# Performance work log

Measured on AMD Instinct MI355X. Metric: run time of the kernel, lower is better.

Reference implementation:

```python
import jax, jax.numpy as jnp
import numpy as np

B, S, D = 2, 2048, 2048
E, TOP_K, H = 8, 2, 1024
HS = 2048  # shared expert ffn dim


def setup_inputs() -> dict:
    key = jax.random.key(0)
    ks = jax.random.split(key, 8)
    sc_d = 1.0 / np.sqrt(D)
    sc_h = 1.0 / np.sqrt(H)
    sc_hs = 1.0 / np.sqrt(HS)
    return {
        "hidden_states": jax.random.normal(ks[0], (B, S, D), jnp.float32),
        "router_w": jax.random.normal(ks[1], (D, E), jnp.float32) * sc_d,
        "w_gate": jax.random.normal(ks[2], (E, D, H), jnp.float32) * sc_d,
        "w_up": jax.random.normal(ks[3], (E, D, H), jnp.float32) * sc_d,
        "w_down": jax.random.normal(ks[4], (E, H, D), jnp.float32) * sc_h,
        "sw_gate": jax.random.normal(ks[5], (D, HS), jnp.float32) * sc_d,
        "sw_up": jax.random.normal(ks[6], (D, HS), jnp.float32) * sc_d,
        "sw_down": jax.random.normal(ks[7], (HS, D), jnp.float32) * sc_hs,
    }


def reference(hidden_states, router_w, w_gate, w_up, w_down, sw_gate, sw_up, sw_down):
    b, s, d = hidden_states.shape
    x = hidden_states.reshape(-1, d)  # [T, D]
    T = x.shape[0]

    # --- gate: softmax router + top-k, renormalized weights ---
    logits = x @ router_w                         # [T, E]
    probs = jax.nn.softmax(logits, axis=-1)
    topk_w, topk_idx = jax.lax.top_k(probs, TOP_K)  # [T, K]
    topk_w = topk_w / jnp.sum(topk_w, axis=-1, keepdims=True)

    # --- routed experts (SwiGLU), dense all-expert compute + sparse combine ---
    g = jnp.einsum('td,edh->teh', x, w_gate)
    u = jnp.einsum('td,edh->teh', x, w_up)
    h = jax.nn.silu(g) * u                        # [T, E, H]
    y = jnp.einsum('teh,ehd->ted', h, w_down)     # [T, E, D]

    # combine weights: scatter top-k weights into [T, E]
    combine = jnp.zeros((T, E), dtype=x.dtype)
    combine = combine.at[jnp.arange(T)[:, None], topk_idx].add(topk_w)
    routed = jnp.einsum('te,ted->td', combine, y)  # [T, D]

    # --- shared expert (SwiGLU) on residual stream ---
    sh = jax.nn.silu(hidden_states @ sw_gate) * (hidden_states @ sw_up)
    shared = sh @ sw_down                          # [B, S, D]

    return routed.reshape(b, s, d) + shared
```

## Files before the change

### kernel.cpp

```cpp
#include <hip/hip_runtime.h>

#define T_TOK 4096
#define DDIM  2048
#define NEXP  8
#define HDIM  1024
#define HSDIM 2048
#define NASSIGN 8192
#define MAXTILES 72

typedef __attribute__((ext_vector_type(8))) short bf16x8;
typedef __attribute__((ext_vector_type(4))) float f32x4;

__device__ __forceinline__ ushort f2bf(float f) {
  union { float f; unsigned u; } v; v.f = f;
  unsigned r = v.u + 0x7FFFu + ((v.u >> 16) & 1u);
  return (ushort)(r >> 16);
}

__device__ __forceinline__ void gload16(const void* g, void* s) {
  __builtin_amdgcn_global_load_lds((const __attribute__((address_space(1))) void*)g,
                                   (__attribute__((address_space(3))) void*)s, 16, 0, 0);
}


__global__ void zero_k(int* ctl) {
  int i = threadIdx.x;
#pragma unroll
  for (int j = 0; j < 4; ++j) ctl[i + j * 256] = 0;
}

__global__ void router_k(const float* __restrict__ x, const float* __restrict__ rw,
                         int* __restrict__ ctl, int* __restrict__ tidx,
                         float* __restrict__ twt) {
  int t = blockIdx.x;
  int lane = threadIdx.x;
  const float* xr = x + (size_t)t * DDIM;
  float acc[NEXP];
#pragma unroll
  for (int e = 0; e < NEXP; ++e) acc[e] = 0.f;
  for (int d0 = lane * 4; d0 < DDIM; d0 += 256) {
    float4 xv = *(const float4*)(xr + d0);
    const float* rwp = rw + (size_t)d0 * NEXP;
#pragma unroll
    for (int e = 0; e < NEXP; ++e)
      acc[e] += xv.x * rwp[e] + xv.y * rwp[NEXP + e] +
                xv.z * rwp[2 * NEXP + e] + xv.w * rwp[3 * NEXP + e];
  }
#pragma unroll
  for (int e = 0; e < NEXP; ++e) {
#pragma unroll
    for (int off = 32; off >= 1; off >>= 1) acc[e] += __shfl_xor(acc[e], off, 64);
  }
  if (lane == 0) {
    int i0 = 0; float m0 = acc[0];
#pragma unroll
    for (int e = 1; e < NEXP; ++e) if (acc[e] > m0) { m0 = acc[e]; i0 = e; }
    int i1 = -1; float m1 = -3.4e38f;
#pragma unroll
    for (int e = 0; e < NEXP; ++e) if (e != i0 && acc[e] > m1) { m1 = acc[e]; i1 = e; }
    float w0 = 1.f / (1.f + __expf(m1 - m0));
    float w1 = 1.f - w0;
    tidx[2 * t] = i0;     twt[2 * t] = w0;
    tidx[2 * t + 1] = i1; twt[2 * t + 1] = w1;
    atomicAdd(&ctl[8 + i0], 1);
    atomicAdd(&ctl[8 + i1], 1);
  }
}

__global__ void plan_k(int* ctl) {
  if (threadIdx.x != 0 || blockIdx.x != 0) return;
  int off = 0, nt = 0;
  for (int e = 0; e < NEXP; ++e) {
    int c = ctl[8 + e];
    ctl[24 + e] = off;
    ctl[16 + e] = off;
    int ntile = (c + 127) >> 7;
    for (int j = 0; j < ntile; ++j) {
      ctl[64 + nt] = e;
      ctl[160 + nt] = off + j * 128;
      ctl[256 + nt] = off + c;
      ++nt;
    }
    off += c;
  }
  ctl[24 + NEXP] = off;
  ctl[0] = nt;
}

__global__ void scatter_k(const int* __restrict__ tidx, const float* __restrict__ twt,
                          int* __restrict__ ctl, int* __restrict__ stok,
                          float* __restrict__ swt) {
  int t = blockIdx.x * blockDim.x + threadIdx.x;
  if (t >= T_TOK) return;
#pragma unroll
  for (int k = 0; k < 2; ++k) {
    int e = tidx[2 * t + k];
    int p = atomicAdd(&ctl[16 + e], 1);
    stok[p] = t;
    swt[p] = twt[2 * t + k];
  }
}

__global__ void cvt_k(const float* __restrict__ in, ushort* __restrict__ out) {
  long long i = ((long long)blockIdx.x * blockDim.x + threadIdx.x) * 8;
  float4 a = *(const float4*)(in + i);
  float4 b = *(const float4*)(in + i + 4);
  ushort4 o0 = { f2bf(a.x), f2bf(a.y), f2bf(a.z), f2bf(a.w) };
  ushort4 o1 = { f2bf(b.x), f2bf(b.y), f2bf(b.z), f2bf(b.w) };
  *(ushort4*)(out + i) = o0;
  *(ushort4*)(out + i + 4) = o1;
}

__global__ void tcvt_k(const float* __restrict__ in, ushort* __restrict__ out,
                       int R, int C) {
  __shared__ float tile[64][65];
  in  += (size_t)blockIdx.z * R * C;
  out += (size_t)blockIdx.z * R * C;
  int c0 = blockIdx.x * 64, r0 = blockIdx.y * 64;
  int tx = threadIdx.x & 15, ty = threadIdx.x >> 4;
#pragma unroll
  for (int i = 0; i < 4; ++i) {
    float4 v = *(const float4*)(in + (size_t)(r0 + ty + 16 * i) * C + c0 + tx * 4);
    tile[ty + 16 * i][tx * 4 + 0] = v.x;
    tile[ty + 16 * i][tx * 4 + 1] = v.y;
    tile[ty + 16 * i][tx * 4 + 2] = v.z;
    tile[ty + 16 * i][tx * 4 + 3] = v.w;
  }
  __syncthreads();
#pragma unroll
  for (int i = 0; i < 4; ++i) {
    ushort4 o = { f2bf(tile[tx * 4 + 0][ty + 16 * i]),
                  f2bf(tile[tx * 4 + 1][ty + 16 * i]),
                  f2bf(tile[tx * 4 + 2][ty + 16 * i]),
                  f2bf(tile[tx * 4 + 3][ty + 16 * i]) };
    *(ushort4*)(out + (size_t)(c0 + ty + 16 * i) * R + r0 + tx * 4) = o;
  }
}

template <bool ROUTED>
__global__ __launch_bounds__(256, 2) void gateup_k(
    const ushort* __restrict__ Ax, const ushort* __restrict__ BgT,
    const ushort* __restrict__ BuT, ushort* __restrict__ Hout,
    const int* __restrict__ ctl, const int* __restrict__ stok, int N) {
  __shared__ ushort As[128 * 32];
  __shared__ ushort Bgs[128 * 32];
  __shared__ ushort Bus[128 * 32];
  __shared__ int toks[128];

  int tid = threadIdx.x;
  int row0, nrows;
  const ushort *Bg, *Bu;
  if (ROUTED) {
    if (blockIdx.x >= ctl[0]) return;
    row0 = ctl[160 + blockIdx.x];
    int end = ctl[256 + blockIdx.x];
    nrows = end - row0; if (nrows > 128) nrows = 128;
    size_t es = (size_t)ctl[64 + blockIdx.x] * HDIM * DDIM;
    Bg = BgT + es; Bu = BuT + es;
    if (tid < 128) toks[tid] = (tid < nrows) ? stok[row0 + tid] : 0;
  } else {
    row0 = blockIdx.x * 128; nrows = 128;
    Bg = BgT; Bu = BuT;
    if (tid < 128) toks[tid] = row0 + tid;
  }
  int col0 = blockIdx.y * 128;
  __syncthreads();

  int srow = tid >> 2, skc = tid & 3;
  const ushort* aS0 = Ax + (size_t)toks[srow] * DDIM + skc * 8;
  const ushort* aS1 = Ax + (size_t)toks[64 + srow] * DDIM + skc * 8;
  const ushort* bgS0 = Bg + (size_t)(col0 + srow) * DDIM + skc * 8;
  const ushort* bgS1 = Bg + (size_t)(col0 + 64 + srow) * DDIM + skc * 8;
  const ushort* buS0 = Bu + (size_t)(col0 + srow) * DDIM + skc * 8;
  const ushort* buS1 = Bu + (size_t)(col0 + 64 + srow) * DDIM + skc * 8;
  ushort* aD0 = As + tid * 8;   ushort* aD1 = As + (256 + tid) * 8;
  ushort* bgD0 = Bgs + tid * 8; ushort* bgD1 = Bgs + (256 + tid) * 8;
  ushort* buD0 = Bus + tid * 8; ushort* buD1 = Bus + (256 + tid) * 8;

  int lane = tid & 63, w = tid >> 6;
  int g = lane >> 4, r16 = lane & 15;
  int wr = (w >> 1) * 64, wc = (w & 1) * 64;

  f32x4 accg[4][4], accu[4][4];
  f32x4 z = {0.f, 0.f, 0.f, 0.f};
#pragma unroll
  for (int i = 0; i < 4; ++i)
#pragma unroll
    for (int j = 0; j < 4; ++j) { accg[i][j] = z; accu[i][j] = z; }

  for (int k0 = 0; k0 < DDIM; k0 += 32) {
    gload16(aS0 + k0, aD0);   gload16(aS1 + k0, aD1);
    gload16(bgS0 + k0, bgD0); gload16(bgS1 + k0, bgD1);
    gload16(buS0 + k0, buD0); gload16(buS1 + k0, buD1);
    __syncthreads();
    bf16x8 af[4], bgf[4], buf_[4];
#pragma unroll
    for (int mf = 0; mf < 4; ++mf)
      af[mf] = *(const bf16x8*)(As + (wr + mf * 16 + r16) * 32 + g * 8);
#pragma unroll
    for (int nf = 0; nf < 4; ++nf) {
      bgf[nf] = *(const bf16x8*)(Bgs + (wc + nf * 16 + r16) * 32 + g * 8);
      buf_[nf] = *(const bf16x8*)(Bus + (wc + nf * 16 + r16) * 32 + g * 8);
    }
#pragma unroll
    for (int mf = 0; mf < 4; ++mf)
#pragma unroll
      for (int nf = 0; nf < 4; ++nf) {
        accg[mf][nf] = __builtin_amdgcn_mfma_f32_16x16x32_bf16(af[mf], bgf[nf], accg[mf][nf], 0, 0, 0);
        accu[mf][nf] = __builtin_amdgcn_mfma_f32_16x16x32_bf16(af[mf], buf_[nf], accu[mf][nf], 0, 0, 0);
      }
    __syncthreads();
  }

#pragma unroll
  for (int mf = 0; mf < 4; ++mf) {
#pragma unroll
    for (int j = 0; j < 4; ++j) {
      int rloc = wr + mf * 16 + g * 4 + j;
      if (rloc < nrows) {
        size_t obase = (size_t)(row0 + rloc) * N + col0 + wc;
#pragma unroll
        for (int nf = 0; nf < 4; ++nf) {
          float gv = accg[mf][nf][j];
          float uv = accu[mf][nf][j];
          float hv = gv / (1.f + __expf(-gv)) * uv;
          Hout[obase + nf * 16 + r16] = f2bf(hv);
        }
      }
    }
  }
}

template <bool ROUTED>
__global__ __launch_bounds__(256, 2) void down_k(
    const ushort* __restrict__ Ah, const ushort* __restrict__ BdT,
    float* __restrict__ Out, const int* __restrict__ ctl,
    const int* __restrict__ stok, const float* __restrict__ swt, int Ktot) {
  __shared__ ushort As[128 * 32];
  __shared__ ushort Bs[128 * 32];
  __shared__ int tokl[128];
  __shared__ float wtl[128];

  int tid = threadIdx.x;
  int row0, nrows;
  const ushort* Bd;
  if (ROUTED) {
    if (blockIdx.x >= ctl[0]) return;
    row0 = ctl[160 + blockIdx.x];
    int end = ctl[256 + blockIdx.x];
    nrows = end - row0; if (nrows > 128) nrows = 128;
    Bd = BdT + (size_t)ctl[64 + blockIdx.x] * DDIM * HDIM;
    if (tid < 128) {
      bool v = tid < nrows;
      tokl[tid] = v ? stok[row0 + tid] : 0;
      wtl[tid] = v ? swt[row0 + tid] : 0.f;
    }
  } else {
    row0 = blockIdx.x * 128; nrows = 128;
    Bd = BdT;
  }
  int col0 = blockIdx.y * 128;
  __syncthreads();

  int srow = tid >> 2, skc = tid & 3;
  const ushort* aS0 = Ah + (size_t)(row0 + srow) * Ktot + skc * 8;
  const ushort* aS1 = Ah + (size_t)(row0 + 64 + srow) * Ktot + skc * 8;
  const ushort* bS0 = Bd + (size_t)(col0 + srow) * Ktot + skc * 8;
  const ushort* bS1 = Bd + (size_t)(col0 + 64 + srow) * Ktot + skc * 8;
  ushort* aD0 = As + tid * 8; ushort* aD1 = As + (256 + tid) * 8;
  ushort* bD0 = Bs + tid * 8; ushort* bD1 = Bs + (256 + tid) * 8;

  int lane = tid & 63, w = tid >> 6;
  int g = lane >> 4, r16 = lane & 15;
  int wr = (w >> 1) * 64, wc = (w & 1) * 64;

  f32x4 acc[4][4];
  f32x4 z = {0.f, 0.f, 0.f, 0.f};
#pragma unroll
  for (int i = 0; i < 4; ++i)
#pragma unroll
    for (int j = 0; j < 4; ++j) acc[i][j] = z;

  for (int k0 = 0; k0 < Ktot; k0 += 32) {
    gload16(aS0 + k0, aD0); gload16(aS1 + k0, aD1);
    gload16(bS0 + k0, bD0); gload16(bS1 + k0, bD1);
    __syncthreads();
    bf16x8 af[4], bf[4];
#pragma unroll
    for (int mf = 0; mf < 4; ++mf)
      af[mf] = *(const bf16x8*)(As + (wr + mf * 16 + r16) * 32 + g * 8);
#pragma unroll
    for (int nf = 0; nf < 4; ++nf)
      bf[nf] = *(const bf16x8*)(Bs + (wc + nf * 16 + r16) * 32 + g * 8);
#pragma unroll
    for (int mf = 0; mf < 4; ++mf)
#pragma unroll
      for (int nf = 0; nf < 4; ++nf)
        acc[mf][nf] = __builtin_amdgcn_mfma_f32_16x16x32_bf16(af[mf], bf[nf], acc[mf][nf], 0, 0, 0);
    __syncthreads();
  }

#pragma unroll
  for (int mf = 0; mf < 4; ++mf) {
#pragma unroll
    for (int j = 0; j < 4; ++j) {
      int rloc = wr + mf * 16 + g * 4 + j;
      if (rloc < nrows) {
        if (ROUTED) {
          int t = tokl[rloc];
          float wt = wtl[rloc];
          size_t obase = (size_t)t * DDIM + col0 + wc;
#pragma unroll
          for (int nf = 0; nf < 4; ++nf)
            atomicAdd(&Out[obase + nf * 16 + r16], wt * acc[mf][nf][j]);
        } else {
          size_t obase = (size_t)(row0 + rloc) * DDIM + col0 + wc;
#pragma unroll
          for (int nf = 0; nf < 4; ++nf)
            Out[obase + nf * 16 + r16] = acc[mf][nf][j];
        }
      }
    }
  }
}

extern "C" void kernel_launch(void* const* d_in, const int* in_sizes, int n_in,
                              void* d_out, int out_size, void* d_ws, size_t ws_size,
                              hipStream_t stream) {
  const float* x   = (const float*)d_in[0];
  const float* rw  = (const float*)d_in[1];
  const float* wg  = (const float*)d_in[2];
  const float* wu  = (const float*)d_in[3];
  const float* wd  = (const float*)d_in[4];
  const float* swg = (const float*)d_in[5];
  const float* swu = (const float*)d_in[6];
  const float* swd = (const float*)d_in[7];
  float* out = (float*)d_out;

  char* ws = (char*)d_ws;
  size_t off = 0;
  auto alloc = [&](size_t bytes) {
    char* p = ws + off;
    off += (bytes + 4095) & ~(size_t)4095;
    return p;
  };
  int*    ctl   = (int*)alloc(4096);
  int*    tidx  = (int*)alloc(NASSIGN * 4);
  float*  twt   = (float*)alloc(NASSIGN * 4);
  int*    stok  = (int*)alloc(NASSIGN * 4);
  float*  swt_  = (float*)alloc(NASSIGN * 4);
  ushort* xbf   = (ushort*)alloc((size_t)T_TOK * DDIM * 2);
  ushort* wgT   = (ushort*)alloc((size_t)NEXP * HDIM * DDIM * 2);
  ushort* wuT   = (ushort*)alloc((size_t)NEXP * HDIM * DDIM * 2);
  ushort* wdT   = (ushort*)alloc((size_t)NEXP * DDIM * HDIM * 2);
  ushort* swgT  = (ushort*)alloc((size_t)HSDIM * DDIM * 2);
  ushort* swuT  = (ushort*)alloc((size_t)HSDIM * DDIM * 2);
  ushort* swdT  = (ushort*)alloc((size_t)DDIM * HSDIM * 2);
  ushort* hbuf  = (ushort*)alloc((size_t)NASSIGN * HDIM * 2);
  ushort* shbuf = (ushort*)alloc((size_t)T_TOK * HSDIM * 2);
  if (off > ws_size) return;

  zero_k<<<1, 256, 0, stream>>>(ctl);
  router_k<<<T_TOK, 64, 0, stream>>>(x, rw, ctl, tidx, twt);
  plan_k<<<1, 64, 0, stream>>>(ctl);
  scatter_k<<<16, 256, 0, stream>>>(tidx, twt, ctl, stok, swt_);

  cvt_k<<<(T_TOK * DDIM / 8) / 256, 256, 0, stream>>>(x, xbf);
  tcvt_k<<<dim3(HDIM / 64, DDIM / 64, NEXP), 256, 0, stream>>>(wg, wgT, DDIM, HDIM);
  tcvt_k<<<dim3(HDIM / 64, DDIM / 64, NEXP), 256, 0, stream>>>(wu, wuT, DDIM, HDIM);
  tcvt_k<<<dim3(DDIM / 64, HDIM / 64, NEXP), 256, 0, stream>>>(wd, wdT, HDIM, DDIM);
  tcvt_k<<<dim3(HSDIM / 64, DDIM / 64, 1), 256, 0, stream>>>(swg, swgT, DDIM, HSDIM);
  tcvt_k<<<dim3(HSDIM / 64, DDIM / 64, 1), 256, 0, stream>>>(swu, swuT, DDIM, HSDIM);
  tcvt_k<<<dim3(DDIM / 64, HSDIM / 64, 1), 256, 0, stream>>>(swd, swdT, HSDIM, DDIM);

  gateup_k<true><<<dim3(MAXTILES, HDIM / 128), 256, 0, stream>>>(xbf, wgT, wuT, hbuf, ctl, stok, HDIM);
  gateup_k<false><<<dim3(T_TOK / 128, HSDIM / 128), 256, 0, stream>>>(xbf, swgT, swuT, shbuf, ctl, stok, HSDIM);
  down_k<false><<<dim3(T_TOK / 128, DDIM / 128), 256, 0, stream>>>(shbuf, swdT, out, ctl, stok, swt_, HSDIM);
  down_k<true><<<dim3(MAXTILES, DDIM / 128), 256, 0, stream>>>(hbuf, wdT, out, ctl, stok, swt_, HDIM);
}
```

Baseline: 802.8 us.

## Use 256x256 double-buffered GEMM tiles with concatenated gate/up weights and XCD swizzle

Gate and up weights are transposed into one concatenated matrix per expert and for the shared expert. A single wider GEMM then writes raw gate/up outputs, and a separate SiLU kernel combines them. GEMM tiles grow to 256x256 with 512 threads, K=64 steps and double-buffered LDS. An XCD-aware workgroup swizzle is added, and routed tiles are planned in 256-row chunks. This aims to raise data reuse and overlap loads with MFMA work. In exchange it adds an extra HBM round trip through the bf16 GU buffer, uses much more LDS per block, and pads more rows in the routed tiles.

```diff
diff --git a/kernel.cpp b/kernel.cpp
--- a/kernel.cpp
+++ b/kernel.cpp
@@ -6,7 +6,7 @@
 #define HDIM  1024
 #define HSDIM 2048
 #define NASSIGN 8192
-#define MAXTILES 72
+#define MAXTILES 40
 
 typedef __attribute__((ext_vector_type(8))) short bf16x8;
 typedef __attribute__((ext_vector_type(4))) float f32x4;
@@ -16,10 +16,18 @@
   unsigned r = v.u + 0x7FFFu + ((v.u >> 16) & 1u);
   return (ushort)(r >> 16);
 }
-
+__device__ __forceinline__ float bf2f(ushort s) {
+  union { float f; unsigned u; } v; v.u = ((unsigned)s) << 16;
+  return v.f;
+}
 __device__ __forceinline__ void gload16(const void* g, void* s) {
   __builtin_amdgcn_global_load_lds((const __attribute__((address_space(1))) void*)g,
                                    (__attribute__((address_space(3))) void*)s, 16, 0, 0);
+}
+__device__ __forceinline__ int xcd_swz(int orig, int nwg) {
+  int q = nwg >> 3, r = nwg & 7;
+  int xcd = orig & 7, pos = orig >> 3;
+  return (xcd < r ? xcd * (q + 1) : r * (q + 1) + (xcd - r) * q) + pos;
 }
 
 
@@ -74,10 +82,10 @@
     int c = ctl[8 + e];
     ctl[24 + e] = off;
     ctl[16 + e] = off;
-    int ntile = (c + 127) >> 7;
+    int ntile = (c + 255) >> 8;
     for (int j = 0; j < ntile; ++j) {
       ctl[64 + nt] = e;
-      ctl[160 + nt] = off + j * 128;
+      ctl[160 + nt] = off + j * 256;
       ctl[256 + nt] = off + c;
       ++nt;
     }
@@ -112,10 +120,10 @@
 }
 
 __global__ void tcvt_k(const float* __restrict__ in, ushort* __restrict__ out,
-                       int R, int C) {
+                       int R, int C, long long inZ, long long outZ) {
   __shared__ float tile[64][65];
-  in  += (size_t)blockIdx.z * R * C;
-  out += (size_t)blockIdx.z * R * C;
+  in  += (size_t)blockIdx.z * inZ;
+  out += (size_t)blockIdx.z * outZ;
   int c0 = blockIdx.x * 64, r0 = blockIdx.y * 64;
   int tx = threadIdx.x & 15, ty = threadIdx.x >> 4;
 #pragma unroll
@@ -137,142 +145,260 @@
   }
 }
 
+__global__ void silu_k(const ushort* __restrict__ gu, ushort* __restrict__ h, int N) {
+  int row = blockIdx.x, c = threadIdx.x * 8;
+  const ushort* gp = gu + (size_t)row * 2 * N;
+  bf16x8 gv = *(const bf16x8*)(gp + c);
+  bf16x8 uv = *(const bf16x8*)(gp + N + c);
+  ushort o[8];
+#pragma unroll
+  for (int k = 0; k < 8; ++k) {
+    float gf = bf2f((ushort)gv[k]);
+    float uf = bf2f((ushort)uv[k]);
+    float hv = gf / (1.f + __expf(-gf)) * uf;
+    o[k] = f2bf(hv);
+  }
+  ushort4 o0 = { o[0], o[1], o[2], o[3] };
+  ushort4 o1 = { o[4], o[5], o[6], o[7] };
+  *(ushort4*)(h + (size_t)row * N + c) = o0;
+  *(ushort4*)(h + (size_t)row * N + c + 4) = o1;
+}
+
 template <bool ROUTED>
-__global__ __launch_bounds__(256, 2) void gateup_k(
-    const ushort* __restrict__ Ax, const ushort* __restrict__ BgT,
-    const ushort* __restrict__ BuT, ushort* __restrict__ Hout,
-    const int* __restrict__ ctl, const int* __restrict__ stok, int N) {
-  __shared__ ushort As[128 * 32];
-  __shared__ ushort Bgs[128 * 32];
-  __shared__ ushort Bus[128 * 32];
-  __shared__ int toks[128];
+__global__ __launch_bounds__(512, 2) void gucat_k(
+    const ushort* __restrict__ Ax, const ushort* __restrict__ Bcat,
+    ushort* __restrict__ GU, const int* __restrict__ ctl,
+    const int* __restrict__ stok, int Ncat) {
+  __shared__ ushort As[2][256 * 64];
+  __shared__ ushort Bs[2][256 * 64];
+  __shared__ int toks[256];
+
+  int nwg = gridDim.x * gridDim.y;
+  int wg = xcd_swz(blockIdx.y * gridDim.x + blockIdx.x, nwg);
+  int mt = wg % gridDim.x, ntt = wg / gridDim.x;
 
   int tid = threadIdx.x;
   int row0, nrows;
-  const ushort *Bg, *Bu;
+  const ushort* Bp;
   if (ROUTED) {
-    if (blockIdx.x >= ctl[0]) return;
-    row0 = ctl[160 + blockIdx.x];
-    int end = ctl[256 + blockIdx.x];
-    nrows = end - row0; if (nrows > 128) nrows = 128;
-    size_t es = (size_t)ctl[64 + blockIdx.x] * HDIM * DDIM;
-    Bg = BgT + es; Bu = BuT + es;
-    if (tid < 128) toks[tid] = (tid < nrows) ? stok[row0 + tid] : 0;
+    if (mt >= ctl[0]) return;
+    row0 = ctl[160 + mt];
+    int end = ctl[256 + mt];
+    nrows = end - row0; if (nrows > 256) nrows = 256;
+    Bp = Bcat + (size_t)ctl[64 + mt] * (2048 * 2048);
+    if (tid < 256) toks[tid] = (tid < nrows) ? stok[row0 + tid] : 0;
   } else {
-    row0 = blockIdx.x * 128; nrows = 128;
-    Bg = BgT; Bu = BuT;
-    if (tid < 128) toks[tid] = row0 + tid;
-  }
-  int col0 = blockIdx.y * 128;
+    row0 = mt * 256; nrows = 256;
+    Bp = Bcat;
+    if (tid < 256) toks[tid] = row0 + tid;
+  }
+  int col0 = ntt * 256;
   __syncthreads();
 
-  int srow = tid >> 2, skc = tid & 3;
-  const ushort* aS0 = Ax + (size_t)toks[srow] * DDIM + skc * 8;
-  const ushort* aS1 = Ax + (size_t)toks[64 + srow] * DDIM + skc * 8;
-  const ushort* bgS0 = Bg + (size_t)(col0 + srow) * DDIM + skc * 8;
-  const ushort* bgS1 = Bg + (size_t)(col0 + 64 + srow) * DDIM + skc * 8;
-  const ushort* buS0 = Bu + (size_t)(col0 + srow) * DDIM + skc * 8;
-  const ushort* buS1 = Bu + (size_t)(col0 + 64 + srow) * DDIM + skc * 8;
-  ushort* aD0 = As + tid * 8;   ushort* aD1 = As + (256 + tid) * 8;
-  ushort* bgD0 = Bgs + tid * 8; ushort* bgD1 = Bgs + (256 + tid) * 8;
-  ushort* buD0 = Bus + tid * 8; ushort* buD1 = Bus + (256 + tid) * 8;
+  int srow = tid >> 3, skc = (tid & 7) * 8;
+  const ushort* aSrc[4];
+  const ushort* bSrc[4];
+#pragma unroll
+  for (int rr = 0; rr < 4; ++rr) {
+    aSrc[rr] = Ax + (size_t)toks[rr * 64 + srow] * DDIM + skc;
+    bSrc[rr] = Bp + (size_t)(col0 + rr * 64 + srow) * DDIM + skc;
+  }
 
   int lane = tid & 63, w = tid >> 6;
   int g = lane >> 4, r16 = lane & 15;
-  int wr = (w >> 1) * 64, wc = (w & 1) * 64;
-
-  f32x4 accg[4][4], accu[4][4];
+  int wrow = (w >> 2) * 128, wcol = (w & 3) * 64;
+
+  f32x4 acc[8][4];
   f32x4 z = {0.f, 0.f, 0.f, 0.f};
 #pragma unroll
-  for (int i = 0; i < 4; ++i)
-#pragma unroll
-    for (int j = 0; j < 4; ++j) { accg[i][j] = z; accu[i][j] = z; }
-
-  for (int k0 = 0; k0 < DDIM; k0 += 32) {
-    gload16(aS0 + k0, aD0);   gload16(aS1 + k0, aD1);
-    gload16(bgS0 + k0, bgD0); gload16(bgS1 + k0, bgD1);
-    gload16(buS0 + k0, buD0); gload16(buS1 + k0, buD1);
+  for (int i = 0; i < 8; ++i)
+#pragma unroll
+    for (int j = 0; j < 4; ++j) acc[i][j] = z;
+
+#define STAGE_GU(buf, k0)                                          \
+  {                                                                 \
+    _Pragma("unroll")                                               \
+    for (int rr = 0; rr < 4; ++rr) {                                \
+      gload16(aSrc[rr] + (k0), &As[buf][(rr * 512 + tid) * 8]);     \
+      gload16(bSrc[rr] + (k0), &Bs[buf][(rr * 512 + tid) * 8]);     \
+    }                                                               \
+  }
+#define COMPUTE_GU(buf)                                                              \
+  {                                                                                   \
+    _Pragma("unroll")                                                                 \
+    for (int kk = 0; kk < 2; ++kk) {                                                  \
+      bf16x8 af[8], bf_[4];                                                           \
+      _Pragma("unroll")                                                               \
+      for (int mf = 0; mf < 8; ++mf)                                                  \
+        af[mf] = *(const bf16x8*)(&As[buf][(wrow + mf * 16 + r16) * 64 + kk * 32 + g * 8]); \
+      _Pragma("unroll")                                                               \
+      for (int nf = 0; nf < 4; ++nf)                                                  \
+        bf_[nf] = *(const bf16x8*)(&Bs[buf][(wcol + nf * 16 + r16) * 64 + kk * 32 + g * 8]); \
+      _Pragma("unroll")                                                               \
+      for (int mf = 0; mf < 8; ++mf)                                                  \
+        _Pragma("unroll")                                                             \
+        for (int nf = 0; nf < 4; ++nf)                                                \
+          acc[mf][nf] = __builtin_amdgcn_mfma_f32_16x16x32_bf16(af[mf], bf_[nf], acc[mf][nf], 0, 0, 0); \
+    }                                                                                 \
+  }
+
+  STAGE_GU(0, 0);
+  __syncthreads();
+  int cur = 0;
+  for (int k0 = 64; k0 < DDIM; k0 += 64) {
+    STAGE_GU(cur ^ 1, k0);
+    COMPUTE_GU(cur);
     __syncthreads();
-    bf16x8 af[4], bgf[4], buf_[4];
-#pragma unroll
-    for (int mf = 0; mf < 4; ++mf)
-      af[mf] = *(const bf16x8*)(As + (wr + mf * 16 + r16) * 32 + g * 8);
-#pragma unroll
-    for (int nf = 0; nf < 4; ++nf) {
-      bgf[nf] = *(const bf16x8*)(Bgs + (wc + nf * 16 + r16) * 32 + g * 8);
-      buf_[nf] = *(const bf16x8*)(Bus + (wc + nf * 16 + r16) * 32 + g * 8);
-    }
-#pragma unroll
-    for (int mf = 0; mf < 4; ++mf)
-#pragma unroll
-      for (int nf = 0; nf < 4; ++nf) {
-        accg[mf][nf] = __builtin_amdgcn_mfma_f32_16x16x32_bf16(af[mf], bgf[nf], accg[mf][nf], 0, 0, 0);
-        accu[mf][nf] = __builtin_amdgcn_mfma_f32_16x16x32_bf16(af[mf], buf_[nf], accu[mf][nf], 0, 0, 0);
-      }
-    __syncthreads();
-  }
-
-#pragma unroll
-  for (int mf = 0; mf < 4; ++mf) {
+    cur ^= 1;
+  }
+  COMPUTE_GU(cur);
+
+#pragma unroll
+  for (int mf = 0; mf < 8; ++mf) {
 #pragma unroll
     for (int j = 0; j < 4; ++j) {
-      int rloc = wr + mf * 16 + g * 4 + j;
+      int rloc = wrow + mf * 16 + g * 4 + j;
       if (rloc < nrows) {
-        size_t obase = (size_t)(row0 + rloc) * N + col0 + wc;
-#pragma unroll
-        for (int nf = 0; nf < 4; ++nf) {
-          float gv = accg[mf][nf][j];
-          float uv = accu[mf][nf][j];
-          float hv = gv / (1.f + __expf(-gv)) * uv;
-          Hout[obase + nf * 16 + r16] = f2bf(hv);
-        }
+        size_t ob = (size_t)(row0 + rloc) * Ncat + col0 + wcol;
+#pragma unroll
+        for (int nf = 0; nf < 4; ++nf)
+          GU[ob + nf * 16 + r16] = f2bf(acc[mf][nf][j]);
       }
     }
   }
-}
-
-template <bool ROUTED>
-__global__ __launch_bounds__(256, 2) void down_k(
+#undef STAGE_GU
+#undef COMPUTE_GU
+}
+
+__global__ __launch_bounds__(512, 2) void downR_k(
     const ushort* __restrict__ Ah, const ushort* __restrict__ BdT,
     float* __restrict__ Out, const int* __restrict__ ctl,
-    const int* __restrict__ stok, const float* __restrict__ swt, int Ktot) {
-  __shared__ ushort As[128 * 32];
-  __shared__ ushort Bs[128 * 32];
-  __shared__ int tokl[128];
-  __shared__ float wtl[128];
+    const int* __restrict__ stok, const float* __restrict__ swt) {
+  __shared__ ushort As[2][256 * 64];
+  __shared__ ushort Bs[2][256 * 64];
+  __shared__ int tokl[256];
+  __shared__ float wtl[256];
+
+  int nwg = gridDim.x * gridDim.y;
+  int wg = xcd_swz(blockIdx.y * gridDim.x + blockIdx.x, nwg);
+  int mt = wg % gridDim.x, ntt = wg / gridDim.x;
 
   int tid = threadIdx.x;
-  int row0, nrows;
-  const ushort* Bd;
-  if (ROUTED) {
-    if (blockIdx.x >= ctl[0]) return;
-    row0 = ctl[160 + blockIdx.x];
-    int end = ctl[256 + blockIdx.x];
-    nrows = end - row0; if (nrows > 128) nrows = 128;
-    Bd = BdT + (size_t)ctl[64 + blockIdx.x] * DDIM * HDIM;
-    if (tid < 128) {
-      bool v = tid < nrows;
-      tokl[tid] = v ? stok[row0 + tid] : 0;
-      wtl[tid] = v ? swt[row0 + tid] : 0.f;
-    }
-  } else {
-    row0 = blockIdx.x * 128; nrows = 128;
-    Bd = BdT;
-  }
-  int col0 = blockIdx.y * 128;
+  if (mt >= ctl[0]) return;
+  int row0 = ctl[160 + mt];
+  int end = ctl[256 + mt];
+  int nrows = end - row0; if (nrows > 256) nrows = 256;
+  const ushort* Bp = BdT + (size_t)ctl[64 + mt] * (2048 * 1024);
+  if (tid < 256) {
+    bool v = tid < nrows;
+    tokl[tid] = v ? stok[row0 + tid] : 0;
+    wtl[tid] = v ? swt[row0 + tid] : 0.f;
+  }
+  int col0 = ntt * 256;
   __syncthreads();
 
-  int srow = tid >> 2, skc = tid & 3;
-  const ushort* aS0 = Ah + (size_t)(row0 + srow) * Ktot + skc * 8;
-  const ushort* aS1 = Ah + (size_t)(row0 + 64 + srow) * Ktot + skc * 8;
-  const ushort* bS0 = Bd + (size_t)(col0 + srow) * Ktot + skc * 8;
-  const ushort* bS1 = Bd + (size_t)(col0 + 64 + srow) * Ktot + skc * 8;
-  ushort* aD0 = As + tid * 8; ushort* aD1 = As + (256 + tid) * 8;
-  ushort* bD0 = Bs + tid * 8; ushort* bD1 = Bs + (256 + tid) * 8;
+  int srow = tid >> 3, skc = (tid & 7) * 8;
+  const ushort* aSrc[4];
+  const ushort* bSrc[4];
+#pragma unroll
+  for (int rr = 0; rr < 4; ++rr) {
+    aSrc[rr] = Ah + (size_t)(row0 + rr * 64 + srow) * HDIM + skc;
+    bSrc[rr] = Bp + (size_t)(col0 + rr * 64 + srow) * HDIM + skc;
+  }
 
   int lane = tid & 63, w = tid >> 6;
   int g = lane >> 4, r16 = lane & 15;
-  int wr = (w >> 1) * 64, wc = (w & 1) * 64;
+  int wrow = (w >> 2) * 128, wcol = (w & 3) * 64;
+
+  f32x4 acc[8][4];
+  f32x4 z = {0.f, 0.f, 0.f, 0.f};
+#pragma unroll
+  for (int i = 0; i < 8; ++i)
+#pragma unroll
+    for (int j = 0; j < 4; ++j) acc[i][j] = z;
+
+#define STAGE_DR(buf, k0)                                          \
+  {                                                                 \
+    _Pragma("unroll")                                               \
+    for (int rr = 0; rr < 4; ++rr) {                                \
+      gload16(aSrc[rr] + (k0), &As[buf][(rr * 512 + tid) * 8]);     \
+      gload16(bSrc[rr] + (k0), &Bs[buf][(rr * 512 + tid) * 8]);     \
+    }                                                               \
+  }
+#define COMPUTE_DR(buf)                                                              \
+  {                                                                                   \
+    _Pragma("unroll")                                                                 \
+    for (int kk = 0; kk < 2; ++kk) {                                                  \
+      bf16x8 af[8], bf_[4];                                                           \
+      _Pragma("unroll")                                                               \
+      for (int mf = 0; mf < 8; ++mf)                                                  \
+        af[mf] = *(const bf16x8*)(&As[buf][(wrow + mf * 16 + r16) * 64 + kk * 32 + g * 8]); \
+      _Pragma("unroll")                                                               \
+      for (int nf = 0; nf < 4; ++nf)                                                  \
+        bf_[nf] = *(const bf16x8*)(&Bs[buf][(wcol + nf * 16 + r16) * 64 + kk * 32 + g * 8]); \
+      _Pragma("unroll")                                                               \
+      for (int mf = 0; mf < 8; ++mf)                                                  \
+        _Pragma("unroll")                                                             \
+        for (int nf = 0; nf < 4; ++nf)                                                \
+          acc[mf][nf] = __builtin_amdgcn_mfma_f32_16x16x32_bf16(af[mf], bf_[nf], acc[mf][nf], 0, 0, 0); \
+    }                                                                                 \
+  }
+
+  STAGE_DR(0, 0);
+  __syncthreads();
+  int cur = 0;
+  for (int k0 = 64; k0 < HDIM; k0 += 64) {
+    STAGE_DR(cur ^ 1, k0);
+    COMPUTE_DR(cur);
+    __syncthreads();
+    cur ^= 1;
+  }
+  COMPUTE_DR(cur);
+
+#pragma unroll
+  for (int mf = 0; mf < 8; ++mf) {
+#pragma unroll
+    for (int j = 0; j < 4; ++j) {
+      int rloc = wrow + mf * 16 + g * 4 + j;
+      if (rloc < nrows) {
+        int t = tokl[rloc];
+        float wt = wtl[rloc];
+        size_t ob = (size_t)t * DDIM + col0 + wcol;
+#pragma unroll
+        for (int nf = 0; nf < 4; ++nf)
+          atomicAdd(&Out[ob + nf * 16 + r16], wt * acc[mf][nf][j]);
+      }
+    }
+  }
+#undef STAGE_DR
+#undef COMPUTE_DR
+}
+
+__global__ __launch_bounds__(512, 2) void downS_k(
+    const ushort* __restrict__ Ah, const ushort* __restrict__ BdT,
+    float* __restrict__ Out) {
+  __shared__ ushort As[2][128 * 64];
+  __shared__ ushort Bs[2][256 * 64];
+
+  int nwg = gridDim.x * gridDim.y;
+  int wg = xcd_swz(blockIdx.y * gridDim.x + blockIdx.x, nwg);
+  int mt = wg % gridDim.x, ntt = wg / gridDim.x;
+  int row0 = mt * 128, col0 = ntt * 256;
+
+  int tid = threadIdx.x;
+  int srow = tid >> 3, skc = (tid & 7) * 8;
+  const ushort* aSrc[2];
+  const ushort* bSrc[4];
+#pragma unroll
+  for (int rr = 0; rr < 2; ++rr)
+    aSrc[rr] = Ah + (size_t)(row0 + rr * 64 + srow) * HSDIM + skc;
+#pragma unroll
+  for (int rr = 0; rr < 4; ++rr)
+    bSrc[rr] = BdT + (size_t)(col0 + rr * 64 + srow) * HSDIM + skc;
+
+  int lane = tid & 63, w = tid >> 6;
+  int g = lane >> 4, r16 = lane & 15;
+  int wrow = (w >> 2) * 64, wcol = (w & 3) * 64;
 
   f32x4 acc[4][4];
   f32x4 z = {0.f, 0.f, 0.f, 0.f};
@@ -281,47 +407,58 @@
 #pragma unroll
     for (int j = 0; j < 4; ++j) acc[i][j] = z;
 
-  for (int k0 = 0; k0 < Ktot; k0 += 32) {
-    gload16(aS0 + k0, aD0); gload16(aS1 + k0, aD1);
-    gload16(bS0 + k0, bD0); gload16(bS1 + k0, bD1);
+#define STAGE_DS(buf, k0)                                          \
+  {                                                                 \
+    _Pragma("unroll")                                               \
+    for (int rr = 0; rr < 2; ++rr)                                  \
+      gload16(aSrc[rr] + (k0), &As[buf][(rr * 512 + tid) * 8]);     \
+    _Pragma("unroll")                                               \
+    for (int rr = 0; rr < 4; ++rr)                                  \
+      gload16(bSrc[rr] + (k0), &Bs[buf][(rr * 512 + tid) * 8]);     \
+  }
+#define COMPUTE_DS(buf)                                                              \
+  {                                                                                   \
+    _Pragma("unroll")                                                                 \
+    for (int kk = 0; kk < 2; ++kk) {                                                  \
+      bf16x8 af[4], bf_[4];                                                           \
+      _Pragma("unroll")                                                               \
+      for (int mf = 0; mf < 4; ++mf)                                                  \
+        af[mf] = *(const bf16x8*)(&As[buf][(wrow + mf * 16 + r16) * 64 + kk * 32 + g * 8]); \
+      _Pragma("unroll")                                                               \
+      for (int nf = 0; nf < 4; ++nf)                                                  \
+        bf_[nf] = *(const bf16x8*)(&Bs[buf][(wcol + nf * 16 + r16) * 64 + kk * 32 + g * 8]); \
+      _Pragma("unroll")                                                               \
+      for (int mf = 0; mf < 4; ++mf)                                                  \
+        _Pragma("unroll")                                                             \
+        for (int nf = 0; nf < 4; ++nf)                                                \
+          acc[mf][nf] = __builtin_amdgcn_mfma_f32_16x16x32_bf16(af[mf], bf_[nf], acc[mf][nf], 0, 0, 0); \
+    }                                                                                 \
+  }
+
+  STAGE_DS(0, 0);
+  __syncthreads();
+  int cur = 0;
+  for (int k0 = 64; k0 < HSDIM; k0 += 64) {
+    STAGE_DS(cur ^ 1, k0);
+    COMPUTE_DS(cur);
     __syncthreads();
-    bf16x8 af[4], bf[4];
-#pragma unroll
-    for (int mf = 0; mf < 4; ++mf)
-      af[mf] = *(const bf16x8*)(As + (wr + mf * 16 + r16) * 32 + g * 8);
-#pragma unroll
-    for (int nf = 0; nf < 4; ++nf)
-      bf[nf] = *(const bf16x8*)(Bs + (wc + nf * 16 + r16) * 32 + g * 8);
-#pragma unroll
-    for (int mf = 0; mf < 4; ++mf)
+    cur ^= 1;
+  }
+  COMPUTE_DS(cur);
+
+#pragma unroll
+  for (int mf = 0; mf < 4; ++mf) {
+#pragma unroll
+    for (int j = 0; j < 4; ++j) {
+      int rloc = wrow + mf * 16 + g * 4 + j;
+      size_t ob = (size_t)(row0 + rloc) * DDIM + col0 + wcol;
 #pragma unroll
       for (int nf = 0; nf < 4; ++nf)
-        acc[mf][nf] = __builtin_amdgcn_mfma_f32_16x16x32_bf16(af[mf], bf[nf], acc[mf][nf], 0, 0, 0);
-    __syncthreads();
-  }
-
-#pragma unroll
-  for (int mf = 0; mf < 4; ++mf) {
-#pragma unroll
-    for (int j = 0; j < 4; ++j) {
-      int rloc = wr + mf * 16 + g * 4 + j;
-      if (rloc < nrows) {
-        if (ROUTED) {
-          int t = tokl[rloc];
-          float wt = wtl[rloc];
-          size_t obase = (size_t)t * DDIM + col0 + wc;
-#pragma unroll
-          for (int nf = 0; nf < 4; ++nf)
-            atomicAdd(&Out[obase + nf * 16 + r16], wt * acc[mf][nf][j]);
-        } else {
-          size_t obase = (size_t)(row0 + rloc) * DDIM + col0 + wc;
-#pragma unroll
-          for (int nf = 0; nf < 4; ++nf)
-            Out[obase + nf * 16 + r16] = acc[mf][nf][j];
-        }
-      }
+        Out[ob + nf * 16 + r16] = acc[mf][nf][j];
     }
   }
+#undef STAGE_DS
+#undef COMPUTE_DS
 }
 
 extern "C" void kernel_launch(void* const* d_in, const int* in_sizes, int n_in,
@@ -350,14 +487,14 @@
   int*    stok  = (int*)alloc(NASSIGN * 4);
   float*  swt_  = (float*)alloc(NASSIGN * 4);
   ushort* xbf   = (ushort*)alloc((size_t)T_TOK * DDIM * 2);
-  ushort* wgT   = (ushort*)alloc((size_t)NEXP * HDIM * DDIM * 2);
-  ushort* wuT   = (ushort*)alloc((size_t)NEXP * HDIM * DDIM * 2);
+  ushort* catR  = (ushort*)alloc((size_t)NEXP * 2048 * 2048 * 2);
   ushort* wdT   = (ushort*)alloc((size_t)NEXP * DDIM * HDIM * 2);
-  ushort* swgT  = (ushort*)alloc((size_t)HSDIM * DDIM * 2);
-  ushort* swuT  = (ushort*)alloc((size_t)HSDIM * DDIM * 2);
+  ushort* catS  = (ushort*)alloc((size_t)2 * HSDIM * DDIM * 2);
   ushort* swdT  = (ushort*)alloc((size_t)DDIM * HSDIM * 2);
-  ushort* hbuf  = (ushort*)alloc((size_t)NASSIGN * HDIM * 2);
-  ushort* shbuf = (ushort*)alloc((size_t)T_TOK * HSDIM * 2);
+  ushort* GU    = (ushort*)alloc((size_t)NASSIGN * 2048 * 2);
+  ushort* hr    = (ushort*)alloc((size_t)(NASSIGN + 256) * HDIM * 2);
+  ushort* hs    = (ushort*)alloc((size_t)T_TOK * HSDIM * 2);
+  (void)alloc(1 << 20);
   if (off > ws_size) return;
 
   zero_k<<<1, 256, 0, stream>>>(ctl);
@@ -366,15 +503,24 @@
   scatter_k<<<16, 256, 0, stream>>>(tidx, twt, ctl, stok, swt_);
 
   cvt_k<<<(T_TOK * DDIM / 8) / 256, 256, 0, stream>>>(x, xbf);
-  tcvt_k<<<dim3(HDIM / 64, DDIM / 64, NEXP), 256, 0, stream>>>(wg, wgT, DDIM, HDIM);
-  tcvt_k<<<dim3(HDIM / 64, DDIM / 64, NEXP), 256, 0, stream>>>(wu, wuT, DDIM, HDIM);
-  tcvt_k<<<dim3(DDIM / 64, HDIM / 64, NEXP), 256, 0, stream>>>(wd, wdT, HDIM, DDIM);
-  tcvt_k<<<dim3(HSDIM / 64, DDIM / 64, 1), 256, 0, stream>>>(swg, swgT, DDIM, HSDIM);
-  tcvt_k<<<dim3(HSDIM / 64, DDIM / 64, 1), 256, 0, stream>>>(swu, swuT, DDIM, HSDIM);
-  tcvt_k<<<dim3(DDIM / 64, HSDIM / 64, 1), 256, 0, stream>>>(swd, swdT, HSDIM, DDIM);
-
-  gateup_k<true><<<dim3(MAXTILES, HDIM / 128), 256, 0, stream>>>(xbf, wgT, wuT, hbuf, ctl, stok, HDIM);
-  gateup_k<false><<<dim3(T_TOK / 128, HSDIM / 128), 256, 0, stream>>>(xbf, swgT, swuT, shbuf, ctl, stok, HSDIM);
-  down_k<false><<<dim3(T_TOK / 128, DDIM / 128), 256, 0, stream>>>(shbuf, swdT, out, ctl, stok, swt_, HSDIM);
-  down_k<true><<<dim3(MAXTILES, DDIM / 128), 256, 0, stream>>>(hbuf, wdT, out, ctl, stok, swt_, HDIM);
-}
+  tcvt_k<<<dim3(HDIM / 64, DDIM / 64, NEXP), 256, 0, stream>>>(
+      wg, catR, DDIM, HDIM, (long long)DDIM * HDIM, 2048LL * 2048);
+  tcvt_k<<<dim3(HDIM / 64, DDIM / 64, NEXP), 256, 0, stream>>>(
+      wu, catR + 1024 * 2048, DDIM, HDIM, (long long)DDIM * HDIM, 2048LL * 2048);
+  tcvt_k<<<dim3(DDIM / 64, HDIM / 64, NEXP), 256, 0, stream>>>(
+      wd, wdT, HDIM, DDIM, (long long)HDIM * DDIM, 2048LL * 1024);
+  tcvt_k<<<dim3(HSDIM / 64, DDIM / 64, 1), 256, 0, stream>>>(
+      swg, catS, DDIM, HSDIM, 0, 0);
+  tcvt_k<<<dim3(HSDIM / 64, DDIM / 64, 1), 256, 0, stream>>>(
+      swu, catS + 2048 * 2048, DDIM, HSDIM, 0, 0);
+  tcvt_k<<<dim3(DDIM / 64, HSDIM / 64, 1), 256, 0, stream>>>(
+      swd, swdT, HSDIM, DDIM, 0, 0);
+
+  gucat_k<true><<<dim3(MAXTILES, 2048 / 256), 512, 0, stream>>>(xbf, catR, GU, ctl, stok, 2048);
+  silu_k<<<NASSIGN, HDIM / 8, 0, stream>>>(GU, hr, HDIM);
+  gucat_k<false><<<dim3(T_TOK / 256, 4096 / 256), 512, 0, stream>>>(xbf, catS, GU, ctl, stok, 4096);
+  silu_k<<<T_TOK, HSDIM / 8, 0, stream>>>(GU, hs, HSDIM);
+
+  downS_k<<<dim3(T_TOK / 128, DDIM / 256), 512, 0, stream>>>(hs, swdT, out);
+  downR_k<<<dim3(MAXTILES, DDIM / 256), 512, 0, stream>>>(hr, wdT, out, ctl, stok, swt_);
+}
```

Result: slower. 923.5 us (+15.0%).

## Double-buffer LDS in GEMMs, swizzle LDS slots, and remap workgroups per XCD

Applied to the files above, without the earlier changes.

The gate/up and down GEMM kernels now use two LDS buffers, so the next K-slice is loaded while the current one is computed, and each iteration needs one barrier instead of two. LDS columns are XOR-swizzled on both the store and the fragment read to cut bank conflicts. Workgroup IDs are remapped so that tiles placed on the same XCD share operands in its L2. down_k's launch bound is raised to 3 waves per SIMD, which puts more pressure on registers, and the double buffers double LDS use.

```diff
diff --git a/kernel.cpp b/kernel.cpp
--- a/kernel.cpp
+++ b/kernel.cpp
@@ -16,10 +16,14 @@
   unsigned r = v.u + 0x7FFFu + ((v.u >> 16) & 1u);
   return (ushort)(r >> 16);
 }
-
 __device__ __forceinline__ void gload16(const void* g, void* s) {
   __builtin_amdgcn_global_load_lds((const __attribute__((address_space(1))) void*)g,
                                    (__attribute__((address_space(3))) void*)s, 16, 0, 0);
+}
+__device__ __forceinline__ int xcd_swz(int orig, int nwg) {
+  int q = nwg >> 3, r = nwg & 7;
+  int xcd = orig & 7, pos = orig >> 3;
+  return (xcd < r ? xcd * (q + 1) : r * (q + 1) + (xcd - r) * q) + pos;
 }
 
 
@@ -112,10 +116,10 @@
 }
 
 __global__ void tcvt_k(const float* __restrict__ in, ushort* __restrict__ out,
-                       int R, int C) {
+                       int R, int C, long long inZ, long long outZ) {
   __shared__ float tile[64][65];
-  in  += (size_t)blockIdx.z * R * C;
-  out += (size_t)blockIdx.z * R * C;
+  in  += (size_t)blockIdx.z * inZ;
+  out += (size_t)blockIdx.z * outZ;
   int c0 = blockIdx.x * 64, r0 = blockIdx.y * 64;
   int tx = threadIdx.x & 15, ty = threadIdx.x >> 4;
 #pragma unroll
@@ -142,43 +146,46 @@
     const ushort* __restrict__ Ax, const ushort* __restrict__ BgT,
     const ushort* __restrict__ BuT, ushort* __restrict__ Hout,
     const int* __restrict__ ctl, const int* __restrict__ stok, int N) {
-  __shared__ ushort As[128 * 32];
-  __shared__ ushort Bgs[128 * 32];
-  __shared__ ushort Bus[128 * 32];
+  __shared__ ushort As[2][128 * 32];
+  __shared__ ushort Bgs[2][128 * 32];
+  __shared__ ushort Bus[2][128 * 32];
   __shared__ int toks[128];
+
+  int nwg = gridDim.x * gridDim.y;
+  int wg = xcd_swz(blockIdx.y * gridDim.x + blockIdx.x, nwg);
+  int mt = wg % gridDim.x, ntt = wg / gridDim.x;
 
   int tid = threadIdx.x;
   int row0, nrows;
   const ushort *Bg, *Bu;
   if (ROUTED) {
-    if (blockIdx.x >= ctl[0]) return;
-    row0 = ctl[160 + blockIdx.x];
-    int end = ctl[256 + blockIdx.x];
+    if (mt >= ctl[0]) return;
+    row0 = ctl[160 + mt];
+    int end = ctl[256 + mt];
     nrows = end - row0; if (nrows > 128) nrows = 128;
-    size_t es = (size_t)ctl[64 + blockIdx.x] * HDIM * DDIM;
+    size_t es = (size_t)ctl[64 + mt] * HDIM * DDIM;
     Bg = BgT + es; Bu = BuT + es;
     if (tid < 128) toks[tid] = (tid < nrows) ? stok[row0 + tid] : 0;
   } else {
-    row0 = blockIdx.x * 128; nrows = 128;
+    row0 = mt * 128; nrows = 128;
     Bg = BgT; Bu = BuT;
     if (tid < 128) toks[tid] = row0 + tid;
   }
-  int col0 = blockIdx.y * 128;
+  int col0 = ntt * 128;
   __syncthreads();
 
-  int srow = tid >> 2, skc = tid & 3;
-  const ushort* aS0 = Ax + (size_t)toks[srow] * DDIM + skc * 8;
-  const ushort* aS1 = Ax + (size_t)toks[64 + srow] * DDIM + skc * 8;
-  const ushort* bgS0 = Bg + (size_t)(col0 + srow) * DDIM + skc * 8;
-  const ushort* bgS1 = Bg + (size_t)(col0 + 64 + srow) * DDIM + skc * 8;
-  const ushort* buS0 = Bu + (size_t)(col0 + srow) * DDIM + skc * 8;
-  const ushort* buS1 = Bu + (size_t)(col0 + 64 + srow) * DDIM + skc * 8;
-  ushort* aD0 = As + tid * 8;   ushort* aD1 = As + (256 + tid) * 8;
-  ushort* bgD0 = Bgs + tid * 8; ushort* bgD1 = Bgs + (256 + tid) * 8;
-  ushort* buD0 = Bus + tid * 8; ushort* buD1 = Bus + (256 + tid) * 8;
+  int srow = tid >> 2;
+  int sslot = (tid & 3) ^ ((tid >> 3) & 3);
+  const ushort* aS0 = Ax + (size_t)toks[srow] * DDIM + sslot * 8;
+  const ushort* aS1 = Ax + (size_t)toks[64 + srow] * DDIM + sslot * 8;
+  const ushort* bgS0 = Bg + (size_t)(col0 + srow) * DDIM + sslot * 8;
+  const ushort* bgS1 = Bg + (size_t)(col0 + 64 + srow) * DDIM + sslot * 8;
+  const ushort* buS0 = Bu + (size_t)(col0 + srow) * DDIM + sslot * 8;
+  const ushort* buS1 = Bu + (size_t)(col0 + 64 + srow) * DDIM + sslot * 8;
 
   int lane = tid & 63, w = tid >> 6;
   int g = lane >> 4, r16 = lane & 15;
+  int xg = (g ^ ((r16 >> 1) & 3)) * 8;
   int wr = (w >> 1) * 64, wc = (w & 1) * 64;
 
   f32x4 accg[4][4], accu[4][4];
@@ -188,29 +195,45 @@
 #pragma unroll
     for (int j = 0; j < 4; ++j) { accg[i][j] = z; accu[i][j] = z; }
 
-  for (int k0 = 0; k0 < DDIM; k0 += 32) {
-    gload16(aS0 + k0, aD0);   gload16(aS1 + k0, aD1);
-    gload16(bgS0 + k0, bgD0); gload16(bgS1 + k0, bgD1);
-    gload16(buS0 + k0, buD0); gload16(buS1 + k0, buD1);
+#define STAGE_GU(buf, k0)                                  \
+  {                                                         \
+    gload16(aS0 + (k0), &As[buf][tid * 8]);                 \
+    gload16(aS1 + (k0), &As[buf][(256 + tid) * 8]);         \
+    gload16(bgS0 + (k0), &Bgs[buf][tid * 8]);               \
+    gload16(bgS1 + (k0), &Bgs[buf][(256 + tid) * 8]);       \
+    gload16(buS0 + (k0), &Bus[buf][tid * 8]);               \
+    gload16(buS1 + (k0), &Bus[buf][(256 + tid) * 8]);       \
+  }
+#define COMPUTE_GU(buf)                                                            \
+  {                                                                                 \
+    bf16x8 af[4], bgf[4], buf_[4];                                                  \
+    _Pragma("unroll")                                                               \
+    for (int mf = 0; mf < 4; ++mf)                                                  \
+      af[mf] = *(const bf16x8*)(&As[buf][(wr + mf * 16 + r16) * 32 + xg]);          \
+    _Pragma("unroll")                                                               \
+    for (int nf = 0; nf < 4; ++nf) {                                                \
+      bgf[nf] = *(const bf16x8*)(&Bgs[buf][(wc + nf * 16 + r16) * 32 + xg]);        \
+      buf_[nf] = *(const bf16x8*)(&Bus[buf][(wc + nf * 16 + r16) * 32 + xg]);       \
+    }                                                                               \
+    _Pragma("unroll")                                                               \
+    for (int mf = 0; mf < 4; ++mf)                                                  \
+      _Pragma("unroll")                                                             \
+      for (int nf = 0; nf < 4; ++nf) {                                              \
+        accg[mf][nf] = __builtin_amdgcn_mfma_f32_16x16x32_bf16(af[mf], bgf[nf], accg[mf][nf], 0, 0, 0); \
+        accu[mf][nf] = __builtin_amdgcn_mfma_f32_16x16x32_bf16(af[mf], buf_[nf], accu[mf][nf], 0, 0, 0); \
+      }                                                                             \
+  }
+
+  STAGE_GU(0, 0);
+  __syncthreads();
+  int cur = 0;
+  for (int k0 = 32; k0 < DDIM; k0 += 32) {
+    STAGE_GU(cur ^ 1, k0);
+    COMPUTE_GU(cur);
     __syncthreads();
-    bf16x8 af[4], bgf[4], buf_[4];
-#pragma unroll
-    for (int mf = 0; mf < 4; ++mf)
-      af[mf] = *(const bf16x8*)(As + (wr + mf * 16 + r16) * 32 + g * 8);
-#pragma unroll
-    for (int nf = 0; nf < 4; ++nf) {
-      bgf[nf] = *(const bf16x8*)(Bgs + (wc + nf * 16 + r16) * 32 + g * 8);
-      buf_[nf] = *(const bf16x8*)(Bus + (wc + nf * 16 + r16) * 32 + g * 8);
-    }
-#pragma unroll
-    for (int mf = 0; mf < 4; ++mf)
-#pragma unroll
-      for (int nf = 0; nf < 4; ++nf) {
-        accg[mf][nf] = __builtin_amdgcn_mfma_f32_16x16x32_bf16(af[mf], bgf[nf], accg[mf][nf], 0, 0, 0);
-        accu[mf][nf] = __builtin_amdgcn_mfma_f32_16x16x32_bf16(af[mf], buf_[nf], accu[mf][nf], 0, 0, 0);
-      }
-    __syncthreads();
-  }
+    cur ^= 1;
+  }
+  COMPUTE_GU(cur);
 
 #pragma unroll
   for (int mf = 0; mf < 4; ++mf) {
@@ -229,49 +252,55 @@
       }
     }
   }
+#undef STAGE_GU
+#undef COMPUTE_GU
 }
 
 template <bool ROUTED>
-__global__ __launch_bounds__(256, 2) void down_k(
+__global__ __launch_bounds__(256, 3) void down_k(
     const ushort* __restrict__ Ah, const ushort* __restrict__ BdT,
     float* __restrict__ Out, const int* __restrict__ ctl,
     const int* __restrict__ stok, const float* __restrict__ swt, int Ktot) {
-  __shared__ ushort As[128 * 32];
-  __shared__ ushort Bs[128 * 32];
+  __shared__ ushort As[2][128 * 32];
+  __shared__ ushort Bs[2][128 * 32];
   __shared__ int tokl[128];
   __shared__ float wtl[128];
+
+  int nwg = gridDim.x * gridDim.y;
+  int wg = xcd_swz(blockIdx.y * gridDim.x + blockIdx.x, nwg);
+  int mt = wg % gridDim.x, ntt = wg / gridDim.x;
 
   int tid = threadIdx.x;
   int row0, nrows;
   const ushort* Bd;
   if (ROUTED) {
-    if (blockIdx.x >= ctl[0]) return;
-    row0 = ctl[160 + blockIdx.x];
-    int end = ctl[256 + blockIdx.x];
+    if (mt >= ctl[0]) return;
+    row0 = ctl[160 + mt];
+    int end = ctl[256 + mt];
     nrows = end - row0; if (nrows > 128) nrows = 128;
-    Bd = BdT + (size_t)ctl[64 + blockIdx.x] * DDIM * HDIM;
+    Bd = BdT + (size_t)ctl[64 + mt] * DDIM * HDIM;
     if (tid < 128) {
       bool v = tid < nrows;
       tokl[tid] = v ? stok[row0 + tid] : 0;
       wtl[tid] = v ? swt[row0 + tid] : 0.f;
     }
   } else {
-    row0 = blockIdx.x * 128; nrows = 128;
+    row0 = mt * 128; nrows = 128;
     Bd = BdT;
   }
-  int col0 = blockIdx.y * 128;
+  int col0 = ntt * 128;
   __syncthreads();
 
-  int srow = tid >> 2, skc = tid & 3;
-  const ushort* aS0 = Ah + (size_t)(row0 + srow) * Ktot + skc * 8;
-  const ushort* aS1 = Ah + (size_t)(row0 + 64 + srow) * Ktot + skc * 8;
-  const ushort* bS0 = Bd + (size_t)(col0 + srow) * Ktot + skc * 8;
-  const ushort* bS1 = Bd + (size_t)(col0 + 64 + srow) * Ktot + skc * 8;
-  ushort* aD0 = As + tid * 8; ushort* aD1 = As + (256 + tid) * 8;
-  ushort* bD0 = Bs + tid * 8; ushort* bD1 = Bs + (256 + tid) * 8;
+  int srow = tid >> 2;
+  int sslot = (tid & 3) ^ ((tid >> 3) & 3);
+  const ushort* aS0 = Ah + (size_t)(row0 + srow) * Ktot + sslot * 8;
+  const ushort* aS1 = Ah + (size_t)(row0 + 64 + srow) * Ktot + sslot * 8;
+  const ushort* bS0 = Bd + (size_t)(col0 + srow) * Ktot + sslot * 8;
+  const ushort* bS1 = Bd + (size_t)(col0 + 64 + srow) * Ktot + sslot * 8;
 
   int lane = tid & 63, w = tid >> 6;
   int g = lane >> 4, r16 = lane & 15;
+  int xg = (g ^ ((r16 >> 1) & 3)) * 8;
   int wr = (w >> 1) * 64, wc = (w & 1) * 64;
 
   f32x4 acc[4][4];
@@ -281,24 +310,39 @@
 #pragma unroll
     for (int j = 0; j < 4; ++j) acc[i][j] = z;
 
-  for (int k0 = 0; k0 < Ktot; k0 += 32) {
-    gload16(aS0 + k0, aD0); gload16(aS1 + k0, aD1);
-    gload16(bS0 + k0, bD0); gload16(bS1 + k0, bD1);
+#define STAGE_D(buf, k0)                                   \
+  {                                                         \
+    gload16(aS0 + (k0), &As[buf][tid * 8]);                 \
+    gload16(aS1 + (k0), &As[buf][(256 + tid) * 8]);         \
+    gload16(bS0 + (k0), &Bs[buf][tid * 8]);                 \
+    gload16(bS1 + (k0), &Bs[buf][(256 + tid) * 8]);         \
+  }
+#define COMPUTE_D(buf)                                                             \
+  {                                                                                 \
+    bf16x8 af[4], bf_[4];                                                           \
+    _Pragma("unroll")                                                               \
+    for (int mf = 0; mf < 4; ++mf)                                                  \
+      af[mf] = *(const bf16x8*)(&As[buf][(wr + mf * 16 + r16) * 32 + xg]);          \
+    _Pragma("unroll")                                                               \
+    for (int nf = 0; nf < 4; ++nf)                                                  \
+      bf_[nf] = *(const bf16x8*)(&Bs[buf][(wc + nf * 16 + r16) * 32 + xg]);         \
+    _Pragma("unroll")                                                               \
+    for (int mf = 0; mf < 4; ++mf)                                                  \
+      _Pragma("unroll")                                                             \
+      for (int nf = 0; nf < 4; ++nf)                                                \
+        acc[mf][nf] = __builtin_amdgcn_mfma_f32_16x16x32_bf16(af[mf], bf_[nf], acc[mf][nf], 0, 0, 0); \
+  }
+
+  STAGE_D(0, 0);
+  __syncthreads();
+  int cur = 0;
+  for (int k0 = 32; k0 < Ktot; k0 += 32) {
+    STAGE_D(cur ^ 1, k0);
+    COMPUTE_D(cur);
     __syncthreads();
-    bf16x8 af[4], bf[4];
-#pragma unroll
-    for (int mf = 0; mf < 4; ++mf)
-      af[mf] = *(const bf16x8*)(As + (wr + mf * 16 + r16) * 32 + g * 8);
-#pragma unroll
-    for (int nf = 0; nf < 4; ++nf)
-      bf[nf] = *(const bf16x8*)(Bs + (wc + nf * 16 + r16) * 32 + g * 8);
-#pragma unroll
-    for (int mf = 0; mf < 4; ++mf)
-#pragma unroll
-      for (int nf = 0; nf < 4; ++nf)
-        acc[mf][nf] = __builtin_amdgcn_mfma_f32_16x16x32_bf16(af[mf], bf[nf], acc[mf][nf], 0, 0, 0);
-    __syncthreads();
-  }
+    cur ^= 1;
+  }
+  COMPUTE_D(cur);
 
 #pragma unroll
   for (int mf = 0; mf < 4; ++mf) {
@@ -322,6 +366,8 @@
       }
     }
   }
+#undef STAGE_D
+#undef COMPUTE_D
 }
 
 extern "C" void kernel_launch(void* const* d_in, const int* in_sizes, int n_in,
@@ -356,8 +402,9 @@
   ushort* swgT  = (ushort*)alloc((size_t)HSDIM * DDIM * 2);
   ushort* swuT  = (ushort*)alloc((size_t)HSDIM * DDIM * 2);
   ushort* swdT  = (ushort*)alloc((size_t)DDIM * HSDIM * 2);
-  ushort* hbuf  = (ushort*)alloc((size_t)NASSIGN * HDIM * 2);
-  ushort* shbuf = (ushort*)alloc((size_t)T_TOK * HSDIM * 2);
+  ushort* hr    = (ushort*)alloc((size_t)(NASSIGN + 256) * HDIM * 2);
+  ushort* hs    = (ushort*)alloc((size_t)T_TOK * HSDIM * 2);
+  (void)alloc(1 << 20);
   if (off > ws_size) return;
 
   zero_k<<<1, 256, 0, stream>>>(ctl);
@@ -366,15 +413,22 @@
   scatter_k<<<16, 256, 0, stream>>>(tidx, twt, ctl, stok, swt_);
 
   cvt_k<<<(T_TOK * DDIM / 8) / 256, 256, 0, stream>>>(x, xbf);
-  tcvt_k<<<dim3(HDIM / 64, DDIM / 64, NEXP), 256, 0, stream>>>(wg, wgT, DDIM, HDIM);
-  tcvt_k<<<dim3(HDIM / 64, DDIM / 64, NEXP), 256, 0, stream>>>(wu, wuT, DDIM, HDIM);
-  tcvt_k<<<dim3(DDIM / 64, HDIM / 64, NEXP), 256, 0, stream>>>(wd, wdT, HDIM, DDIM);
-  tcvt_k<<<dim3(HSDIM / 64, DDIM / 64, 1), 256, 0, stream>>>(swg, swgT, DDIM, HSDIM);
-  tcvt_k<<<dim3(HSDIM / 64, DDIM / 64, 1), 256, 0, stream>>>(swu, swuT, DDIM, HSDIM);
-  tcvt_k<<<dim3(DDIM / 64, HSDIM / 64, 1), 256, 0, stream>>>(swd, swdT, HSDIM, DDIM);
-
-  gateup_k<true><<<dim3(MAXTILES, HDIM / 128), 256, 0, stream>>>(xbf, wgT, wuT, hbuf, ctl, stok, HDIM);
-  gateup_k<false><<<dim3(T_TOK / 128, HSDIM / 128), 256, 0, stream>>>(xbf, swgT, swuT, shbuf, ctl, stok, HSDIM);
-  down_k<false><<<dim3(T_TOK / 128, DDIM / 128), 256, 0, stream>>>(shbuf, swdT, out, ctl, stok, swt_, HSDIM);
-  down_k<true><<<dim3(MAXTILES, DDIM / 128), 256, 0, stream>>>(hbuf, wdT, out, ctl, stok, swt_, HDIM);
-}
+  tcvt_k<<<dim3(HDIM / 64, DDIM / 64, NEXP), 256, 0, stream>>>(
+      wg, wgT, DDIM, HDIM, (long long)DDIM * HDIM, (long long)HDIM * DDIM);
+  tcvt_k<<<dim3(HDIM / 64, DDIM / 64, NEXP), 256, 0, stream>>>(
+      wu, wuT, DDIM, HDIM, (long long)DDIM * HDIM, (long long)HDIM * DDIM);
+  tcvt_k<<<dim3(DDIM / 64, HDIM / 64, NEXP), 256, 0, stream>>>(
+      wd, wdT, HDIM, DDIM, (long long)HDIM * DDIM, (long long)DDIM * HDIM);
+  tcvt_k<<<dim3(HSDIM / 64, DDIM / 64, 1), 256, 0, stream>>>(
+      swg, swgT, DDIM, HSDIM, 0, 0);
+  tcvt_k<<<dim3(HSDIM / 64, DDIM / 64, 1), 256, 0, stream>>>(
+      swu, swuT, DDIM, HSDIM, 0, 0);
+  tcvt_k<<<dim3(DDIM / 64, HSDIM / 64, 1), 256, 0, stream>>>(
+      swd, swdT, HSDIM, DDIM, 0, 0);
+
+  gateup_k<true><<<dim3(MAXTILES, HDIM / 128), 256, 0, stream>>>(xbf, wgT, wuT, hr, ctl, stok, HDIM);
+  gateup_k<false><<<dim3(T_TOK / 128, HSDIM / 128), 256, 0, stream>>>(xbf, swgT, swuT, hs, ctl, stok, HSDIM);
+
+  down_k<false><<<dim3(T_TOK / 128, DDIM / 128), 256, 0, stream>>>(hs, swdT, out, ctl, stok, swt_, HSDIM);
+  down_k<true><<<dim3(MAXTILES, DDIM / 128), 256, 0, stream>>>(hr, wdT, out, ctl, stok, swt_, HDIM);
+}
```

Measured after the change: 841.2 us. 1.05x slower.
